# Performance work log

Hardware: AMD Instinct MI355X
Metric: run time of the kernel (lower is better)

The kernel has to match this reference:

```python
import jax, jax.numpy as jnp
import numpy as np

NUM_GRAPHS = 64


def gcn_conv(x, edge_index, W, b):
    # PyG GCNConv: x' = D^-1/2 (A+I) D^-1/2 (x W) + b, self-loops added.
    n = x.shape[0]
    h = x @ W  # [N, out]
    loop = jnp.arange(n)
    src = jnp.concatenate([edge_index[0], loop])
    dst = jnp.concatenate([edge_index[1], loop])
    deg = jax.ops.segment_sum(jnp.ones_like(dst, dtype=h.dtype), dst, num_segments=n)
    dinv = jnp.where(deg > 0, jax.lax.rsqrt(deg), 0.0)
    norm = dinv[src] * dinv[dst]  # [E+N]
    msgs = h[src] * norm[:, None]  # gather + scale
    out = jax.ops.segment_sum(msgs, dst, num_segments=n)  # scatter-add
    return out + b


def lstm_step(x, W_ih, W_hh, b_ih, b_hh):
    # single time step, zero initial state; PyTorch gate order i,f,g,o
    H = W_hh.shape[1]
    gates = x @ W_ih.T + b_ih + b_hh  # h0 = 0 so W_hh term vanishes
    i, f, g, o = jnp.split(gates, 4, axis=-1)
    i, f, o = jax.nn.sigmoid(i), jax.nn.sigmoid(f), jax.nn.sigmoid(o)
    c = i * jnp.tanh(g)  # f * c0 = 0
    return o * jnp.tanh(c)


def setup_inputs() -> dict:
    key = jax.random.key(0)
    ks = jax.random.split(key, 16)
    N, E, F, G, H, C = 50000, 600000, 128, 128, 256, 1
    s = lambda *sh: 1.0 / np.sqrt(sh[-1])
    return {
        "x": jax.random.normal(ks[0], (N, F), jnp.float32),
        "edge_index": jax.random.randint(ks[1], (2, E), 0, N),
        "batch": jnp.sort(jax.random.randint(ks[2], (N,), 0, NUM_GRAPHS)),
        "W1": jax.random.normal(ks[3], (F, G), jnp.float32) * s(F, G),
        "b1": jnp.zeros((G,), jnp.float32),
        "W2": jax.random.normal(ks[4], (G, G), jnp.float32) * s(G, G),
        "b2": jnp.zeros((G,), jnp.float32),
        "W_ih": jax.random.normal(ks[5], (4 * H, G), jnp.float32) * s(4 * H, G),
        "W_hh": jax.random.normal(ks[6], (4 * H, H), jnp.float32) * s(4 * H, H),
        "b_ih": jnp.zeros((4 * H,), jnp.float32),
        "b_hh": jnp.zeros((4 * H,), jnp.float32),
        "Wm": jax.random.normal(ks[7], (C, H), jnp.float32) * s(C, H),
        "bm": jnp.zeros((C,), jnp.float32),
        "Wv": jax.random.normal(ks[8], (C, H), jnp.float32) * s(C, H),
        "bv": jnp.zeros((C,), jnp.float32),
    }


def reference(x, edge_index, batch, W1, b1, W2, b2, W_ih, W_hh, b_ih, b_hh, Wm, bm, Wv, bv):
    h = jax.nn.relu(gcn_conv(x, edge_index, W1, b1))
    h = jax.nn.relu(gcn_conv(h, edge_index, W2, b2))
    # global mean pool over graphs
    sums = jax.ops.segment_sum(h, batch, num_segments=NUM_GRAPHS)
    cnts = jax.ops.segment_sum(jnp.ones_like(batch, dtype=h.dtype), batch, num_segments=NUM_GRAPHS)
    pooled = sums / jnp.maximum(cnts, 1.0)[:, None]  # [G_graphs, gcn_hidden]
    hT = lstm_step(pooled, W_ih, W_hh, b_ih, b_hh)  # [G_graphs, lstm_hidden]
    mean = hT @ Wm.T + bm
    log_var = jax.nn.softplus(hT @ Wv.T + bv)
    return (mean, log_var)
```

## Files before the change

### kernel.cpp

```cpp
#include <hip/hip_runtime.h>
#include <hip/hip_bf16.h>
#include <math.h>


#define POOL_SUB 32

typedef __attribute__((ext_vector_type(8))) short bf16x8;
typedef __attribute__((ext_vector_type(4))) float f32x4;

static __device__ __forceinline__ unsigned short f2bf(float f) {
    union { float f; unsigned int u; } v; v.f = f;
    unsigned int u = v.u;
    unsigned int r = u + 0x7FFFu + ((u >> 16) & 1u);
    return (unsigned short)(r >> 16);
}
static __device__ __forceinline__ unsigned int pack2bf(float lo, float hi) {
    return (unsigned int)f2bf(lo) | ((unsigned int)f2bf(hi) << 16);
}
static __device__ __forceinline__ float bflo(unsigned int v) {
    union { unsigned int u; float f; } w; w.u = v << 16; return w.f;
}
static __device__ __forceinline__ float bfhi(unsigned int v) {
    union { unsigned int u; float f; } w; w.u = v & 0xFFFF0000u; return w.f;
}

__global__ void count_deg_kernel(const int* __restrict__ dst, int E, int* __restrict__ deg) {
    int e = blockIdx.x * blockDim.x + threadIdx.x;
    if (e < E) atomicAdd(&deg[dst[e]], 1);
}

__global__ void scan_pass1(const int* __restrict__ deg, int n,
                           int* __restrict__ rowptr, int* __restrict__ bsums) {
    __shared__ int s[256];
    int tid = threadIdx.x;
    int base = blockIdx.x * 1024;
    int v[4];
    int mysum = 0;
#pragma unroll
    for (int j = 0; j < 4; ++j) {
        int idx = base + tid * 4 + j;
        v[j] = (idx < n) ? deg[idx] : 0;
        mysum += v[j];
    }
    s[tid] = mysum;
    __syncthreads();
    for (int off = 1; off < 256; off <<= 1) {
        int t = (tid >= off) ? s[tid - off] : 0;
        __syncthreads();
        s[tid] += t;
        __syncthreads();
    }
    int excl = s[tid] - mysum;
#pragma unroll
    for (int j = 0; j < 4; ++j) {
        int idx = base + tid * 4 + j;
        if (idx < n) rowptr[idx] = excl;
        excl += v[j];
    }
    if (tid == 255) bsums[blockIdx.x] = s[255];
}

__global__ void scan_pass2(int* bsums, int nb) {
    __shared__ int s[64];
    int tid = threadIdx.x;
    int v = (tid < nb) ? bsums[tid] : 0;
    s[tid] = v;
    __syncthreads();
    for (int off = 1; off < 64; off <<= 1) {
        int t = (tid >= off) ? s[tid - off] : 0;
        __syncthreads();
        s[tid] += t;
        __syncthreads();
    }
    if (tid < nb) bsums[tid] = s[tid] - v;
    if (tid == 63) bsums[nb] = s[63];
}

__global__ void scan_pass3(int* __restrict__ rowptr, const int* __restrict__ bsums, int n, int nb) {
    int tid = threadIdx.x;
    int base = blockIdx.x * 1024;
    int add = bsums[blockIdx.x];
#pragma unroll
    for (int j = 0; j < 4; ++j) {
        int idx = base + tid * 4 + j;
        if (idx < n) rowptr[idx] += add;
    }
    if (blockIdx.x == 0 && tid == 0) rowptr[n] = bsums[nb];
}

__global__ void fill_csr_kernel(const int* __restrict__ src, const int* __restrict__ dst, int E,
                                const int* __restrict__ rowptr, int* __restrict__ cursor,
                                int* __restrict__ csr) {
    int e = blockIdx.x * blockDim.x + threadIdx.x;
    if (e < E) {
        int d = dst[e];
        int pos = rowptr[d] + atomicAdd(&cursor[d], 1);
        csr[pos] = src[e];
    }
}

__global__ void dinv_kernel(const int* __restrict__ deg, float* __restrict__ dinv, int n) {
    int i = blockIdx.x * blockDim.x + threadIdx.x;
    if (i < n) dinv[i] = rsqrtf((float)deg[i] + 1.0f);
}

__global__ void xcvt_kernel(const float* __restrict__ x, unsigned int* __restrict__ xb, int total4) {
    int i = blockIdx.x * blockDim.x + threadIdx.x;
    if (i < total4) {
        float4 v = ((const float4*)x)[i];
        ((uint2*)xb)[i] = make_uint2(pack2bf(v.x, v.y), pack2bf(v.z, v.w));
    }
}

__global__ void wcvt_kernel(const float* __restrict__ W1, const float* __restrict__ W2,
                            unsigned short* __restrict__ Wt1, unsigned short* __restrict__ Wt2) {
    int nb = blockIdx.x & 127;
    const float* Ws = (blockIdx.x < 128) ? W1 : W2;
    unsigned short* Wd = (blockIdx.x < 128) ? Wt1 : Wt2;
    int k = threadIdx.x;
    Wd[nb * 128 + k] = f2bf(Ws[(size_t)k * 128 + nb]);
}

__global__ __launch_bounds__(256) void gemm_mfma_kernel(const unsigned short* __restrict__ A,
                                                        const unsigned short* __restrict__ Wt,
                                                        const float* __restrict__ dinv,
                                                        unsigned short* __restrict__ out,
                                                        int n) {
    int tid = threadIdx.x;
    int l = tid & 63;
    int wid = tid >> 6;
    int rowbase = blockIdx.x * 64 + wid * 16;
    int lc = l & 15;
    int kq = l >> 4;

    int arow = rowbase + lc; if (arow > n - 1) arow = n - 1;
    const unsigned short* Ap = A + (size_t)arow * 128 + kq * 8;
    const unsigned short* Wp = Wt + (size_t)lc * 128 + kq * 8;

    f32x4 acc[8];
#pragma unroll
    for (int c = 0; c < 8; ++c) acc[c] = (f32x4){0.f, 0.f, 0.f, 0.f};

#pragma unroll
    for (int ks = 0; ks < 4; ++ks) {
        bf16x8 a = *(const bf16x8*)(Ap + ks * 32);
#pragma unroll
        for (int c = 0; c < 8; ++c) {
            bf16x8 b = *(const bf16x8*)(Wp + c * 2048 + ks * 32);
            acc[c] = __builtin_amdgcn_mfma_f32_16x16x32_bf16(a, b, acc[c], 0, 0, 0);
        }
    }

    int r0 = kq * 4;
    float s[4];
    int orow[4];
#pragma unroll
    for (int r = 0; r < 4; ++r) {
        orow[r] = rowbase + r0 + r;
        s[r] = (orow[r] < n) ? dinv[orow[r]] : 0.f;
    }
#pragma unroll
    for (int c = 0; c < 8; ++c) {
#pragma unroll
        for (int r = 0; r < 4; ++r) {
            if (orow[r] < n)
                out[(size_t)orow[r] * 128 + c * 16 + lc] = f2bf(acc[c][r] * s[r]);
        }
    }
}

__global__ __launch_bounds__(256) void aggregate_kernel(const unsigned int* __restrict__ g,
                                                        const int* __restrict__ rowptr,
                                                        const int* __restrict__ csr,
                                                        const float* __restrict__ dinv,
                                                        const float* __restrict__ bias,
                                                        unsigned int* __restrict__ out, int n) {
    int lane = threadIdx.x & 63;
    int node = (blockIdx.x * blockDim.x + threadIdx.x) >> 6;
    if (node >= n) return;
    int beg = rowptr[node], end = rowptr[node + 1];
    unsigned int sv = g[(size_t)node * 64 + lane];
    float ax = bflo(sv), ay = bfhi(sv);
    int e = beg;
    for (; e + 4 <= end; e += 4) {
        int s0 = csr[e + 0], s1 = csr[e + 1], s2 = csr[e + 2], s3 = csr[e + 3];
        unsigned int v0 = g[(size_t)s0 * 64 + lane];
        unsigned int v1 = g[(size_t)s1 * 64 + lane];
        unsigned int v2 = g[(size_t)s2 * 64 + lane];
        unsigned int v3 = g[(size_t)s3 * 64 + lane];
        ax += bflo(v0) + bflo(v1) + bflo(v2) + bflo(v3);
        ay += bfhi(v0) + bfhi(v1) + bfhi(v2) + bfhi(v3);
    }
    for (; e < end; ++e) {
        unsigned int v0 = g[(size_t)csr[e] * 64 + lane];
        ax += bflo(v0);
        ay += bfhi(v0);
    }
    float dv = dinv[node];
    float2 b = ((const float2*)bias)[lane];
    float rx = fmaxf(dv * ax + b.x, 0.f);
    float ry = fmaxf(dv * ay + b.y, 0.f);
    out[(size_t)node * 64 + lane] = pack2bf(rx, ry);
}

__global__ __launch_bounds__(64) void pool_partial_kernel(const unsigned int* __restrict__ h,
                                                          const int* __restrict__ batch, int n,
                                                          float* __restrict__ partial) {
    int g = blockIdx.x / POOL_SUB;
    int sub = blockIdx.x % POOL_SUB;
    int t = threadIdx.x;
    int lo = 0, hi = n;
    while (lo < hi) { int mid = (lo + hi) >> 1; if (batch[mid] < g) lo = mid + 1; else hi = mid; }
    int start = lo;
    hi = n;
    while (lo < hi) { int mid = (lo + hi) >> 1; if (batch[mid] < g + 1) lo = mid + 1; else hi = mid; }
    int end = lo;
    int len = end - start;
    int b0 = start + (int)((long long)len * sub / POOL_SUB);
    int b1 = start + (int)((long long)len * (sub + 1) / POOL_SUB);
    float ax = 0.f, ay = 0.f;
    int i = b0;
    for (; i + 4 <= b1; i += 4) {
        unsigned int v0 = h[(size_t)(i + 0) * 64 + t];
        unsigned int v1 = h[(size_t)(i + 1) * 64 + t];
        unsigned int v2 = h[(size_t)(i + 2) * 64 + t];
        unsigned int v3 = h[(size_t)(i + 3) * 64 + t];
        ax += bflo(v0) + bflo(v1) + bflo(v2) + bflo(v3);
        ay += bfhi(v0) + bfhi(v1) + bfhi(v2) + bfhi(v3);
    }
    for (; i < b1; ++i) {
        unsigned int v0 = h[(size_t)i * 64 + t];
        ax += bflo(v0);
        ay += bfhi(v0);
    }
    partial[(size_t)blockIdx.x * 128 + 2 * t]     = ax;
    partial[(size_t)blockIdx.x * 128 + 2 * t + 1] = ay;
}

__global__ __launch_bounds__(128) void pool_finish_kernel(const float* __restrict__ partial,
                                                          const int* __restrict__ batch, int n,
                                                          float* __restrict__ pooled) {
    int g = blockIdx.x;
    int tid = threadIdx.x;
    int lo = 0, hi = n;
    while (lo < hi) { int mid = (lo + hi) >> 1; if (batch[mid] < g) lo = mid + 1; else hi = mid; }
    int start = lo;
    hi = n;
    while (lo < hi) { int mid = (lo + hi) >> 1; if (batch[mid] < g + 1) lo = mid + 1; else hi = mid; }
    int end = lo;
    float acc = 0.f;
#pragma unroll
    for (int s = 0; s < POOL_SUB; ++s)
        acc += partial[(size_t)(g * POOL_SUB + s) * 128 + tid];
    pooled[g * 128 + tid] = acc / fmaxf((float)(end - start), 1.0f);
}

__global__ __launch_bounds__(256) void lstm_head_kernel(const float* __restrict__ pooled,
                                                        const float* __restrict__ W_ih,
                                                        const float* __restrict__ b_ih,
                                                        const float* __restrict__ b_hh,
                                                        const float* __restrict__ Wm,
                                                        const float* __restrict__ bm,
                                                        const float* __restrict__ Wv,
                                                        const float* __restrict__ bv,
                                                        float* __restrict__ out) {
    __shared__ __align__(16) float p[128];
    __shared__ float redm[256];
    __shared__ float redv[256];
    int gph = blockIdx.x;
    int tid = threadIdx.x;
    if (tid < 128) p[tid] = pooled[gph * 128 + tid];
    __syncthreads();
    float gi = b_ih[tid] + b_hh[tid];
    float gg = b_ih[512 + tid] + b_hh[512 + tid];
    float go = b_ih[768 + tid] + b_hh[768 + tid];
    const float4* wi = (const float4*)(W_ih + (size_t)tid * 128);
    const float4* wg = (const float4*)(W_ih + (size_t)(512 + tid) * 128);
    const float4* wo = (const float4*)(W_ih + (size_t)(768 + tid) * 128);
    const float4* p4 = (const float4*)p;
#pragma unroll 8
    for (int k = 0; k < 32; ++k) {
        float4 xv = p4[k];
        float4 a = wi[k], bq = wg[k], cq = wo[k];
        gi += xv.x * a.x + xv.y * a.y + xv.z * a.z + xv.w * a.w;
        gg += xv.x * bq.x + xv.y * bq.y + xv.z * bq.z + xv.w * bq.w;
        go += xv.x * cq.x + xv.y * cq.y + xv.z * cq.z + xv.w * cq.w;
    }
    float iv = 1.f / (1.f + expf(-gi));
    float cv = iv * tanhf(gg);
    float ov = 1.f / (1.f + expf(-go));
    float hT = ov * tanhf(cv);
    redm[tid] = hT * Wm[tid];
    redv[tid] = hT * Wv[tid];
    __syncthreads();
    for (int s = 128; s > 0; s >>= 1) {
        if (tid < s) { redm[tid] += redm[tid + s]; redv[tid] += redv[tid + s]; }
        __syncthreads();
    }
    if (tid == 0) {
        out[gph] = redm[0] + bm[0];
        float xv = redv[0] + bv[0];
        out[64 + gph] = fmaxf(xv, 0.f) + log1pf(expf(-fabsf(xv)));
    }
}

extern "C" void kernel_launch(void* const* d_in, const int* in_sizes, int n_in,
                              void* d_out, int out_size, void* d_ws, size_t ws_size,
                              hipStream_t stream) {
    const float* x     = (const float*)d_in[0];
    const int*   edge  = (const int*)d_in[1];
    const int*   batch = (const int*)d_in[2];
    const float* W1    = (const float*)d_in[3];
    const float* b1    = (const float*)d_in[4];
    const float* W2    = (const float*)d_in[5];
    const float* b2    = (const float*)d_in[6];
    const float* W_ih  = (const float*)d_in[7];
    const float* b_ih  = (const float*)d_in[9];
    const float* b_hh  = (const float*)d_in[10];
    const float* Wm    = (const float*)d_in[11];
    const float* bm    = (const float*)d_in[12];
    const float* Wv    = (const float*)d_in[13];
    const float* bv    = (const float*)d_in[14];
    float* out = (float*)d_out;

    const int N = in_sizes[0] / 128;
    const int E = in_sizes[1] / 2;
    const int* srcIdx = edge;
    const int* dstIdx = edge + E;

    char* ws = (char*)d_ws;
    size_t off = 0;
    const size_t gB = (size_t)N * 64 * sizeof(unsigned int);
    unsigned int* gbuf = (unsigned int*)(ws + off); off += gB;
    unsigned int* hbuf = (unsigned int*)(ws + off); off += gB;
    unsigned int* xb   = (unsigned int*)(ws + off); off += gB;
    int* deg    = (int*)(ws + off);   off += (size_t)N * sizeof(int);
    int* cursor = (int*)(ws + off);   off += (size_t)N * sizeof(int);
    int* rowptr = (int*)(ws + off);   off += (size_t)(N + 1) * sizeof(int);
    off = (off + 255) & ~(size_t)255;
    int* bsums  = (int*)(ws + off);   off += 512;
    int* csr    = (int*)(ws + off);   off += (size_t)E * sizeof(int);
    off = (off + 255) & ~(size_t)255;
    float* dinv = (float*)(ws + off); off += (size_t)N * sizeof(float);
    off = (off + 255) & ~(size_t)255;
    unsigned short* Wt1 = (unsigned short*)(ws + off); off += 128 * 128 * sizeof(unsigned short);
    unsigned short* Wt2 = (unsigned short*)(ws + off); off += 128 * 128 * sizeof(unsigned short);
    off = (off + 255) & ~(size_t)255;
    float* pooled = (float*)(ws + off); off += 64 * 128 * sizeof(float);
    off = (off + 255) & ~(size_t)255;
    float* partial = (float*)(ws + off); off += (size_t)64 * POOL_SUB * 128 * sizeof(float);

    hipMemsetAsync(deg, 0, (size_t)2 * N * sizeof(int), stream);

    xcvt_kernel<<<(N * 32 + 255) / 256, 256, 0, stream>>>(x, xb, N * 32);
    wcvt_kernel<<<256, 128, 0, stream>>>(W1, W2, Wt1, Wt2);

    int eb = (E + 255) / 256;
    count_deg_kernel<<<eb, 256, 0, stream>>>(dstIdx, E, deg);

    int nb = (N + 1023) / 1024;
    scan_pass1<<<nb, 256, 0, stream>>>(deg, N, rowptr, bsums);
    scan_pass2<<<1, 64, 0, stream>>>(bsums, nb);
    scan_pass3<<<nb, 256, 0, stream>>>(rowptr, bsums, N, nb);
    dinv_kernel<<<(N + 255) / 256, 256, 0, stream>>>(deg, dinv, N);
    fill_csr_kernel<<<eb, 256, 0, stream>>>(srcIdx, dstIdx, E, rowptr, cursor, csr);

    int gb = (N + 63) / 64;
    int ab = (N + 3) / 4;

    gemm_mfma_kernel<<<gb, 256, 0, stream>>>(xb ? (const unsigned short*)xb : 0, Wt1, dinv, (unsigned short*)gbuf, N);
    aggregate_kernel<<<ab, 256, 0, stream>>>(gbuf, rowptr, csr, dinv, b1, hbuf, N);
    gemm_mfma_kernel<<<gb, 256, 0, stream>>>((const unsigned short*)hbuf, Wt2, dinv, (unsigned short*)gbuf, N);
    aggregate_kernel<<<ab, 256, 0, stream>>>(gbuf, rowptr, csr, dinv, b2, hbuf, N);

    pool_partial_kernel<<<64 * POOL_SUB, 64, 0, stream>>>(hbuf, batch, N, partial);
    pool_finish_kernel<<<64, 128, 0, stream>>>(partial, batch, N, pooled);
    lstm_head_kernel<<<64, 256, 0, stream>>>(pooled, W_ih, b_ih, b_hh, Wm, bm, Wv, bv, out);
}
```

Baseline: 230.2 us.

## Fuse small kernels: f32 input conversion into GEMM, dinv into scan, pool into LSTM

```diff
diff --git a/kernel.cpp b/kernel.cpp
--- a/kernel.cpp
+++ b/kernel.cpp
@@ -22,6 +22,19 @@
 }
 static __device__ __forceinline__ float bfhi(unsigned int v) {
     union { unsigned int u; float f; } w; w.u = v & 0xFFFF0000u; return w.f;
+}
+static __device__ __forceinline__ bf16x8 f8_to_bf(float4 f0, float4 f1) {
+    union { unsigned int u[4]; bf16x8 v; } r;
+    r.u[0] = pack2bf(f0.x, f0.y);
+    r.u[1] = pack2bf(f0.z, f0.w);
+    r.u[2] = pack2bf(f1.x, f1.y);
+    r.u[3] = pack2bf(f1.z, f1.w);
+    return r.v;
+}
+
+__global__ void zero_kernel(int* __restrict__ p, int n) {
+    int i = blockIdx.x * blockDim.x + threadIdx.x;
+    if (i < n) p[i] = 0;
 }
 
 __global__ void count_deg_kernel(const int* __restrict__ dst, int E, int* __restrict__ deg) {
@@ -76,14 +89,19 @@
     if (tid == 63) bsums[nb] = s[63];
 }
 
-__global__ void scan_pass3(int* __restrict__ rowptr, const int* __restrict__ bsums, int n, int nb) {
+__global__ void scan_pass3(int* __restrict__ rowptr, const int* __restrict__ bsums,
+                           const int* __restrict__ deg, float* __restrict__ dinv,
+                           int n, int nb) {
     int tid = threadIdx.x;
     int base = blockIdx.x * 1024;
     int add = bsums[blockIdx.x];
 #pragma unroll
     for (int j = 0; j < 4; ++j) {
         int idx = base + tid * 4 + j;
-        if (idx < n) rowptr[idx] += add;
+        if (idx < n) {
+            rowptr[idx] += add;
+            dinv[idx] = rsqrtf((float)deg[idx] + 1.0f);
+        }
     }
     if (blockIdx.x == 0 && tid == 0) rowptr[n] = bsums[nb];
 }
@@ -99,19 +117,6 @@
     }
 }
 
-__global__ void dinv_kernel(const int* __restrict__ deg, float* __restrict__ dinv, int n) {
-    int i = blockIdx.x * blockDim.x + threadIdx.x;
-    if (i < n) dinv[i] = rsqrtf((float)deg[i] + 1.0f);
-}
-
-__global__ void xcvt_kernel(const float* __restrict__ x, unsigned int* __restrict__ xb, int total4) {
-    int i = blockIdx.x * blockDim.x + threadIdx.x;
-    if (i < total4) {
-        float4 v = ((const float4*)x)[i];
-        ((uint2*)xb)[i] = make_uint2(pack2bf(v.x, v.y), pack2bf(v.z, v.w));
-    }
-}
-
 __global__ void wcvt_kernel(const float* __restrict__ W1, const float* __restrict__ W2,
                             unsigned short* __restrict__ Wt1, unsigned short* __restrict__ Wt2) {
     int nb = blockIdx.x & 127;
@@ -119,6 +124,56 @@
     unsigned short* Wd = (blockIdx.x < 128) ? Wt1 : Wt2;
     int k = threadIdx.x;
     Wd[nb * 128 + k] = f2bf(Ws[(size_t)k * 128 + nb]);
+}
+
+__global__ __launch_bounds__(256) void gemm_mfma_f32a_kernel(const float* __restrict__ A,
+                                                             const unsigned short* __restrict__ Wt,
+                                                             const float* __restrict__ dinv,
+                                                             unsigned short* __restrict__ out,
+                                                             int n) {
+    int tid = threadIdx.x;
+    int l = tid & 63;
+    int wid = tid >> 6;
+    int rowbase = blockIdx.x * 64 + wid * 16;
+    int lc = l & 15;
+    int kq = l >> 4;
+
+    int arow = rowbase + lc; if (arow > n - 1) arow = n - 1;
+    const float* Ap = A + (size_t)arow * 128 + kq * 8;
+    const unsigned short* Wp = Wt + (size_t)lc * 128 + kq * 8;
+
+    f32x4 acc[8];
+#pragma unroll
+    for (int c = 0; c < 8; ++c) acc[c] = (f32x4){0.f, 0.f, 0.f, 0.f};
+
+#pragma unroll
+    for (int ks = 0; ks < 4; ++ks) {
+        float4 f0 = *(const float4*)(Ap + ks * 32);
+        float4 f1 = *(const float4*)(Ap + ks * 32 + 4);
+        bf16x8 a = f8_to_bf(f0, f1);
+#pragma unroll
+        for (int c = 0; c < 8; ++c) {
+            bf16x8 b = *(const bf16x8*)(Wp + c * 2048 + ks * 32);
+            acc[c] = __builtin_amdgcn_mfma_f32_16x16x32_bf16(a, b, acc[c], 0, 0, 0);
+        }
+    }
+
+    int r0 = kq * 4;
+    float s[4];
+    int orow[4];
+#pragma unroll
+    for (int r = 0; r < 4; ++r) {
+        orow[r] = rowbase + r0 + r;
+        s[r] = (orow[r] < n) ? dinv[orow[r]] : 0.f;
+    }
+#pragma unroll
+    for (int c = 0; c < 8; ++c) {
+#pragma unroll
+        for (int r = 0; r < 4; ++r) {
+            if (orow[r] < n)
+                out[(size_t)orow[r] * 128 + c * 16 + lc] = f2bf(acc[c][r] * s[r]);
+        }
+    }
 }
 
 __global__ __launch_bounds__(256) void gemm_mfma_kernel(const unsigned short* __restrict__ A,
@@ -237,25 +292,8 @@
     partial[(size_t)blockIdx.x * 128 + 2 * t + 1] = ay;
 }
 
-__global__ __launch_bounds__(128) void pool_finish_kernel(const float* __restrict__ partial,
-                                                          const int* __restrict__ batch, int n,
-                                                          float* __restrict__ pooled) {
-    int g = blockIdx.x;
-    int tid = threadIdx.x;
-    int lo = 0, hi = n;
-    while (lo < hi) { int mid = (lo + hi) >> 1; if (batch[mid] < g) lo = mid + 1; else hi = mid; }
-    int start = lo;
-    hi = n;
-    while (lo < hi) { int mid = (lo + hi) >> 1; if (batch[mid] < g + 1) lo = mid + 1; else hi = mid; }
-    int end = lo;
-    float acc = 0.f;
-#pragma unroll
-    for (int s = 0; s < POOL_SUB; ++s)
-        acc += partial[(size_t)(g * POOL_SUB + s) * 128 + tid];
-    pooled[g * 128 + tid] = acc / fmaxf((float)(end - start), 1.0f);
-}
-
-__global__ __launch_bounds__(256) void lstm_head_kernel(const float* __restrict__ pooled,
+__global__ __launch_bounds__(256) void pool_lstm_kernel(const float* __restrict__ partial,
+                                                        const int* __restrict__ batch, int n,
                                                         const float* __restrict__ W_ih,
                                                         const float* __restrict__ b_ih,
                                                         const float* __restrict__ b_hh,
@@ -269,7 +307,19 @@
     __shared__ float redv[256];
     int gph = blockIdx.x;
     int tid = threadIdx.x;
-    if (tid < 128) p[tid] = pooled[gph * 128 + tid];
+    if (tid < 128) {
+        int lo = 0, hi = n;
+        while (lo < hi) { int mid = (lo + hi) >> 1; if (batch[mid] < gph) lo = mid + 1; else hi = mid; }
+        int start = lo;
+        hi = n;
+        while (lo < hi) { int mid = (lo + hi) >> 1; if (batch[mid] < gph + 1) lo = mid + 1; else hi = mid; }
+        int end = lo;
+        float acc = 0.f;
+#pragma unroll
+        for (int s = 0; s < POOL_SUB; ++s)
+            acc += partial[(size_t)(gph * POOL_SUB + s) * 128 + tid];
+        p[tid] = acc / fmaxf((float)(end - start), 1.0f);
+    }
     __syncthreads();
     float gi = b_ih[tid] + b_hh[tid];
     float gg = b_ih[512 + tid] + b_hh[512 + tid];
@@ -333,7 +383,6 @@
     const size_t gB = (size_t)N * 64 * sizeof(unsigned int);
     unsigned int* gbuf = (unsigned int*)(ws + off); off += gB;
     unsigned int* hbuf = (unsigned int*)(ws + off); off += gB;
-    unsigned int* xb   = (unsigned int*)(ws + off); off += gB;
     int* deg    = (int*)(ws + off);   off += (size_t)N * sizeof(int);
     int* cursor = (int*)(ws + off);   off += (size_t)N * sizeof(int);
     int* rowptr = (int*)(ws + off);   off += (size_t)(N + 1) * sizeof(int);
@@ -346,13 +395,10 @@
     unsigned short* Wt1 = (unsigned short*)(ws + off); off += 128 * 128 * sizeof(unsigned short);
     unsigned short* Wt2 = (unsigned short*)(ws + off); off += 128 * 128 * sizeof(unsigned short);
     off = (off + 255) & ~(size_t)255;
-    float* pooled = (float*)(ws + off); off += 64 * 128 * sizeof(float);
-    off = (off + 255) & ~(size_t)255;
     float* partial = (float*)(ws + off); off += (size_t)64 * POOL_SUB * 128 * sizeof(float);
 
-    hipMemsetAsync(deg, 0, (size_t)2 * N * sizeof(int), stream);
-
-    xcvt_kernel<<<(N * 32 + 255) / 256, 256, 0, stream>>>(x, xb, N * 32);
+    zero_kernel<<<(2 * N + 255) / 256, 256, 0, stream>>>(deg, 2 * N);
+
     wcvt_kernel<<<256, 128, 0, stream>>>(W1, W2, Wt1, Wt2);
 
     int eb = (E + 255) / 256;
@@ -361,19 +407,17 @@
     int nb = (N + 1023) / 1024;
     scan_pass1<<<nb, 256, 0, stream>>>(deg, N, rowptr, bsums);
     scan_pass2<<<1, 64, 0, stream>>>(bsums, nb);
-    scan_pass3<<<nb, 256, 0, stream>>>(rowptr, bsums, N, nb);
-    dinv_kernel<<<(N + 255) / 256, 256, 0, stream>>>(deg, dinv, N);
+    scan_pass3<<<nb, 256, 0, stream>>>(rowptr, bsums, deg, dinv, N, nb);
     fill_csr_kernel<<<eb, 256, 0, stream>>>(srcIdx, dstIdx, E, rowptr, cursor, csr);
 
     int gb = (N + 63) / 64;
     int ab = (N + 3) / 4;
 
-    gemm_mfma_kernel<<<gb, 256, 0, stream>>>(xb ? (const unsigned short*)xb : 0, Wt1, dinv, (unsigned short*)gbuf, N);
+    gemm_mfma_f32a_kernel<<<gb, 256, 0, stream>>>(x, Wt1, dinv, (unsigned short*)gbuf, N);
     aggregate_kernel<<<ab, 256, 0, stream>>>(gbuf, rowptr, csr, dinv, b1, hbuf, N);
     gemm_mfma_kernel<<<gb, 256, 0, stream>>>((const unsigned short*)hbuf, Wt2, dinv, (unsigned short*)gbuf, N);
     aggregate_kernel<<<ab, 256, 0, stream>>>(gbuf, rowptr, csr, dinv, b2, hbuf, N);
 
     pool_partial_kernel<<<64 * POOL_SUB, 64, 0, stream>>>(hbuf, batch, N, partial);
-    pool_finish_kernel<<<64, 128, 0, stream>>>(partial, batch, N, pooled);
-    lstm_head_kernel<<<64, 256, 0, stream>>>(pooled, W_ih, b_ih, b_hh, Wm, bm, Wv, bv, out);
-}
+    pool_lstm_kernel<<<64, 256, 0, stream>>>(partial, batch, N, W_ih, b_ih, b_hh, Wm, bm, Wv, bv, out);
+}
```

New measurement: 222.3 us. -3.4%, faster.
